# Kernel optimization log

Measured on AMD Instinct MI355X. Metric: run time of the kernel, lower is better.

## Reference

```python
import jax, jax.numpy as jnp
import numpy as np
from jax import lax

BN_EPS = 1e-5
LN_EPS = 1e-5
EPS = 1e-6


def _bn(x, g, b, m, v):
    inv = g / jnp.sqrt(v + BN_EPS)
    return (x - m[None, :, None, None]) * inv[None, :, None, None] + b[None, :, None, None]


def _conv1x1(x, w, b=None):
    y = jnp.einsum('bchw,oc->bohw', x, w)
    if b is not None:
        y = y + b[None, :, None, None]
    return y


def _conv2d(x, w, pad_h, pad_w):
    return lax.conv_general_dilated(x, w, (1, 1), [(pad_h, pad_h), (pad_w, pad_w)],
                                    dimension_numbers=('NCHW', 'OIHW', 'NCHW'))


def _haar_dwt(x):
    # Haar analysis, stride-2: pure 2x2 add/sub arithmetic (H, W assumed even).
    B, C, H, W = x.shape
    xb = x.reshape(B, C, H // 2, 2, W // 2, 2)
    x00 = xb[:, :, :, 0, :, 0]; x01 = xb[:, :, :, 0, :, 1]
    x10 = xb[:, :, :, 1, :, 0]; x11 = xb[:, :, :, 1, :, 1]
    LL = 0.5 * (x00 + x01 + x10 + x11)
    LH = 0.5 * (-x00 + x01 - x10 + x11)
    HL = 0.5 * (-x00 - x01 + x10 + x11)
    HH = 0.5 * (x00 - x01 - x10 + x11)
    return LH, HL, HH, LL


def _haar_idwt(LH, HL, HH, LL):
    # Matches conv_transpose2d(stride=2) with the same Haar kernels.
    x00 = 0.5 * (LL - LH - HL + HH); x01 = 0.5 * (LL + LH - HL - HH)
    x10 = 0.5 * (LL - LH + HL - HH); x11 = 0.5 * (LL + LH + HL + HH)
    B, C, h, w = LL.shape
    top = jnp.stack([x00, x01], axis=-1)  # (B,C,h,w,2)
    bot = jnp.stack([x10, x11], axis=-1)
    y = jnp.stack([top, bot], axis=3)     # (B,C,h,2,w,2)
    return y.reshape(B, C, 2 * h, 2 * w)


def _soft_threshold(x, thr):
    return jnp.sign(x) * jax.nn.relu(jnp.abs(x) - thr)


def _forward(x, red_w, red_bias, red_bn_g, red_bn_b, red_bn_m, red_bn_v,
             gct_fc1_w, gct_fc1_b, gct_ln_g, gct_ln_b, gct_fc2_w, gct_fc2_b,
             rel_h_w, rel_h_b, rel_h_bn_g, rel_h_bn_b, rel_h_bn_m, rel_h_bn_v,
             rel_v_w, rel_v_b, rel_v_bn_g, rel_v_bn_b, rel_v_bn_m, rel_v_bn_v,
             rel_fus_w, rel_fus_b, hw_theta, hw_fuse_w, hw_fc_w, hw_fc_b,
             sf_w, sf_b, sf_bn_g, sf_bn_b, sf_bn_m, sf_bn_v, fin_w, fin_b):
    B, C, H, W = x.shape
    split = C // 2  # alpha = 0.5
    identity = x[:, :split]
    gate = x[:, split:]
    r = jax.nn.relu(_bn(_conv1x1(gate, red_w, red_bias), red_bn_g, red_bn_b, red_bn_m, red_bn_v))
    # --- GCT stream: GAP -> Linear -> LayerNorm -> ReLU -> Linear -> sigmoid gate ---
    ctx = r.mean(axis=(2, 3))                      # (B,Cr)
    h1 = ctx @ gct_fc1_w.T + gct_fc1_b
    mu = h1.mean(-1, keepdims=True)
    var = ((h1 - mu) ** 2).mean(-1, keepdims=True)
    h1 = (h1 - mu) / jnp.sqrt(var + LN_EPS) * gct_ln_g + gct_ln_b
    w_gct = jax.nn.sigmoid(jax.nn.relu(h1) @ gct_fc2_w.T + gct_fc2_b)
    gct_out = r * w_gct[:, :, None, None]
    # --- Rel stream: anisotropic pool -> conv/BN/ReLU -> bilinear(size-1 axis == broadcast) ---
    hf = _conv2d(r.mean(axis=2, keepdims=True), rel_h_w, 0, 1) + rel_h_b[None, :, None, None]
    hf = jax.nn.relu(_bn(hf, rel_h_bn_g, rel_h_bn_b, rel_h_bn_m, rel_h_bn_v))
    hf = jnp.broadcast_to(hf, (B, hf.shape[1], H, W))
    vf = _conv2d(r.mean(axis=3, keepdims=True), rel_v_w, 1, 0) + rel_v_b[None, :, None, None]
    vf = jax.nn.relu(_bn(vf, rel_v_bn_g, rel_v_bn_b, rel_v_bn_m, rel_v_bn_v))
    vf = jnp.broadcast_to(vf, (B, vf.shape[1], H, W))
    rel_w_map = jax.nn.sigmoid(_conv1x1(jnp.concatenate([hf, vf], axis=1), rel_fus_w, rel_fus_b))
    rel_out = r * rel_w_map
    # --- HWFE / wavelet attention ---
    LH, HL, HH, LL = _haar_dwt(r)
    t = jax.nn.sigmoid(hw_theta)                   # (3,Cr,1,1)
    m_LH = jnp.abs(LH).mean(axis=(2, 3), keepdims=True) + EPS
    m_HL = jnp.abs(HL).mean(axis=(2, 3), keepdims=True) + EPS
    m_HH = jnp.abs(HH).mean(axis=(2, 3), keepdims=True) + EPS
    LH_h = _soft_threshold(LH, t[0][None] * m_LH)
    HL_h = _soft_threshold(HL, t[1][None] * m_HL)
    HH_h = _soft_threshold(HH, t[2][None] * m_HH)
    fused = _conv1x1(jnp.concatenate([LH_h, HL_h, HH_h], axis=1), hw_fuse_w)
    X_re = _haar_idwt(LH_h, HL_h, fused, LL)       # note: fused sits in HH slot, as in source
    gap = X_re.mean(axis=(2, 3)) @ hw_fc_w.T + hw_fc_b
    attn = jax.nn.softmax(gap, axis=1)
    hwfe_out = r * attn[:, :, None, None]
    # --- stream fusion + gating ---
    interaction = gct_out * rel_out + hwfe_out
    gate_weight = jax.nn.sigmoid(_bn(_conv1x1(interaction, sf_w, sf_b), sf_bn_g, sf_bn_b, sf_bn_m, sf_bn_v))
    out = jnp.concatenate([identity, gate * gate_weight], axis=1)
    return _conv1x1(out, fin_w, fin_b)


def setup_inputs() -> dict:
    key = jax.random.key(0)
    ks = jax.random.split(key, 20)
    B, C, H, W = 16, 512, 64, 64
    Cg = C // 2           # gate channels = 256
    Cr = 16               # max(4, 256 // 16)
    Ch = Cr // 2          # 8
    Hd = max(1, Cr // 4)  # 4
    f = lambda k, s: jax.random.normal(k, s, jnp.float32) * 0.05
    return dict(
        x=jax.random.normal(ks[0], (B, C, H, W), jnp.float32),
        red_w=f(ks[1], (Cr, Cg)), red_bias=f(ks[2], (Cr,)),
        red_bn_g=jnp.ones((Cr,)), red_bn_b=jnp.zeros((Cr,)),
        red_bn_m=jnp.zeros((Cr,)), red_bn_v=jnp.ones((Cr,)),
        gct_fc1_w=f(ks[3], (Hd, Cr)), gct_fc1_b=f(ks[4], (Hd,)),
        gct_ln_g=jnp.ones((Hd,)), gct_ln_b=jnp.zeros((Hd,)),
        gct_fc2_w=f(ks[5], (Cr, Hd)), gct_fc2_b=f(ks[6], (Cr,)),
        rel_h_w=f(ks[7], (Ch, Cr, 1, 3)), rel_h_b=f(ks[8], (Ch,)),
        rel_h_bn_g=jnp.ones((Ch,)), rel_h_bn_b=jnp.zeros((Ch,)),
        rel_h_bn_m=jnp.zeros((Ch,)), rel_h_bn_v=jnp.ones((Ch,)),
        rel_v_w=f(ks[9], (Ch, Cr, 3, 1)), rel_v_b=f(ks[10], (Ch,)),
        rel_v_bn_g=jnp.ones((Ch,)), rel_v_bn_b=jnp.zeros((Ch,)),
        rel_v_bn_m=jnp.zeros((Ch,)), rel_v_bn_v=jnp.ones((Ch,)),
        rel_fus_w=f(ks[11], (Cr, 2 * Ch)), rel_fus_b=f(ks[12], (Cr,)),
        hw_theta=f(ks[13], (3, Cr, 1, 1)), hw_fuse_w=f(ks[14], (Cr, 3 * Cr)),
        hw_fc_w=f(ks[15], (Cr, Cr)), hw_fc_b=f(ks[16], (Cr,)),
        sf_w=f(ks[17], (Cg, Cr)), sf_b=f(ks[18], (Cg,)),
        sf_bn_g=jnp.ones((Cg,)), sf_bn_b=jnp.zeros((Cg,)),
        sf_bn_m=jnp.zeros((Cg,)), sf_bn_v=jnp.ones((Cg,)),
        fin_w=f(ks[19], (C, C)), fin_b=jnp.zeros((C,)),
    )


def reference(x, red_w, red_bias, red_bn_g, red_bn_b, red_bn_m, red_bn_v,
              gct_fc1_w, gct_fc1_b, gct_ln_g, gct_ln_b, gct_fc2_w, gct_fc2_b,
              rel_h_w, rel_h_b, rel_h_bn_g, rel_h_bn_b, rel_h_bn_m, rel_h_bn_v,
              rel_v_w, rel_v_b, rel_v_bn_g, rel_v_bn_b, rel_v_bn_m, rel_v_bn_v,
              rel_fus_w, rel_fus_b, hw_theta, hw_fuse_w, hw_fc_w, hw_fc_b,
              sf_w, sf_b, sf_bn_g, sf_bn_b, sf_bn_m, sf_bn_v, fin_w, fin_b):
    return _forward(x, red_w, red_bias, red_bn_g, red_bn_b, red_bn_m, red_bn_v,
                    gct_fc1_w, gct_fc1_b, gct_ln_g, gct_ln_b, gct_fc2_w, gct_fc2_b,
                    rel_h_w, rel_h_b, rel_h_bn_g, rel_h_bn_b, rel_h_bn_m, rel_h_bn_v,
                    rel_v_w, rel_v_b, rel_v_bn_g, rel_v_bn_b, rel_v_bn_m, rel_v_bn_v,
                    rel_fus_w, rel_fus_b, hw_theta, hw_fuse_w, hw_fc_w, hw_fc_b,
                    sf_w, sf_b, sf_bn_g, sf_bn_b, sf_bn_m, sf_bn_v, fin_w, fin_b)
```

## Files before the change

kernel.cpp:

```cpp
#include <hip/hip_runtime.h>
#include <cstdint>

typedef uint16_t u16;
typedef uint32_t u32;
typedef uint64_t u64;
typedef __attribute__((ext_vector_type(4))) float f32x4;
typedef __attribute__((ext_vector_type(8))) short bf16x8;

__device__ __forceinline__ u16 f2bf(float f) {
  union { float f; u32 i; } u; u.f = f;
  u32 r = u.i + 0x7FFFu + ((u.i >> 16) & 1u);
  return (u16)(r >> 16);
}
__device__ __forceinline__ float sigm(float x) { return 1.f / (1.f + __expf(-x)); }

__global__ __launch_bounds__(256, 4) void k1_reduce(
    const float* __restrict__ x, const float* __restrict__ rw, const float* __restrict__ rb,
    const float* __restrict__ bg, const float* __restrict__ bb, const float* __restrict__ bm,
    const float* __restrict__ bv, float* __restrict__ r)
{
  __shared__ __align__(16) float wl[256][16];
  __shared__ float bl[16];
  __shared__ float sl[16];
  __shared__ float sc[4][64][17];
  int t = threadIdx.x;
  if (t < 16) {
    float s = bg[t] * rsqrtf(bv[t] + 1e-5f);
    sl[t] = s;
    bl[t] = (rb[t] - bm[t]) * s + bb[t];
  }
  __syncthreads();
  for (int i = 0; i < 16; ++i) {
    int flat = i * 256 + t;
    int co = flat >> 8, c = flat & 255;
    wl[c][co] = rw[co * 256 + c] * sl[co];
  }
  __syncthreads();
  int g = t >> 6, l = t & 63;
  int pg = blockIdx.x * 64 + l;
  int b = pg >> 12, pp = pg & 4095;
  const float* gsrc = x + ((size_t)(b * 512 + 256 + g * 64)) * 4096 + pp;
  float acc[16];
#pragma unroll
  for (int co = 0; co < 16; ++co) acc[co] = 0.f;
#pragma unroll 8
  for (int c = 0; c < 64; ++c) {
    float gv = gsrc[(size_t)c * 4096];
    const f32x4* wr = (const f32x4*)(&wl[g * 64 + c][0]);
    f32x4 a0 = wr[0], a1 = wr[1], a2 = wr[2], a3 = wr[3];
    acc[0]  += gv * a0[0]; acc[1]  += gv * a0[1]; acc[2]  += gv * a0[2]; acc[3]  += gv * a0[3];
    acc[4]  += gv * a1[0]; acc[5]  += gv * a1[1]; acc[6]  += gv * a1[2]; acc[7]  += gv * a1[3];
    acc[8]  += gv * a2[0]; acc[9]  += gv * a2[1]; acc[10] += gv * a2[2]; acc[11] += gv * a2[3];
    acc[12] += gv * a3[0]; acc[13] += gv * a3[1]; acc[14] += gv * a3[2]; acc[15] += gv * a3[3];
  }
#pragma unroll
  for (int co = 0; co < 16; ++co) sc[g][l][co] = acc[co];
  __syncthreads();
  int ppb = (blockIdx.x * 64) & 4095;
#pragma unroll
  for (int i = 0; i < 4; ++i) {
    int idx = i * 256 + t;
    int l2 = idx & 63, co = idx >> 6;
    float s = sc[0][l2][co] + sc[1][l2][co] + sc[2][l2][co] + sc[3][l2][co] + bl[co];
    r[((size_t)(b * 16 + co)) * 4096 + ppb + l2] = fmaxf(s, 0.f);
  }
}

__global__ __launch_bounds__(256) void k2_means(
    const float* __restrict__ r, float* __restrict__ cm, float* __restrict__ rm,
    float* __restrict__ ctx)
{
  __shared__ __align__(16) float tile[64][68];
  int bc = blockIdx.x, t = threadIdx.x;
  const float* src = r + (size_t)bc * 4096;
#pragma unroll
  for (int i = 0; i < 4; ++i) {
    int off = (i * 256 + t) * 4;
    int row = off >> 6, col = off & 63;
    f32x4 v = *(const f32x4*)(src + off);
    *(f32x4*)&tile[row][col] = v;
  }
  __syncthreads();
  int wv = t >> 6, lane = t & 63;
  if (wv == 0) {
    float s = 0.f;
    for (int h = 0; h < 64; ++h) s += tile[h][lane];
    cm[bc * 64 + lane] = s * (1.f / 64.f);
    float tot = s;
#pragma unroll
    for (int m = 32; m; m >>= 1) tot += __shfl_xor(tot, m, 64);
    if (lane == 0) ctx[bc] = tot * (1.f / 4096.f);
  } else if (wv == 1) {
    float s = 0.f;
    for (int w0 = 0; w0 < 64; ++w0) s += tile[lane][(w0 + lane) & 63];
    rm[bc * 64 + lane] = s * (1.f / 64.f);
  }
}

__global__ __launch_bounds__(256) void k3x(
    const float* __restrict__ finw, u16* __restrict__ fwb,
    const float* __restrict__ ctx,
    const float* f1w, const float* f1b, const float* lng, const float* lnb,
    const float* f2w, const float* f2b, const float* fcw, const float* fcb,
    float* __restrict__ wgct, float* __restrict__ attn,
    const float* __restrict__ cm, const float* __restrict__ rm,
    const float* hw, const float* hb, const float* hbg, const float* hbb, const float* hbm, const float* hbv,
    const float* vw, const float* vb_, const float* vbg, const float* vbb, const float* vbm, const float* vbv,
    const float* fw, const float* fb, float* __restrict__ hfc, float* __restrict__ vfc)
{
  int bid = blockIdx.x, t = threadIdx.x;
  if (bid < 256) {
    int i = bid * 256 + t;
    f32x4 v = ((const f32x4*)finw)[i];
    u64 p = (u64)f2bf(v[0]) | ((u64)f2bf(v[1]) << 16) |
            ((u64)f2bf(v[2]) << 32) | ((u64)f2bf(v[3]) << 48);
    ((u64*)fwb)[i] = p;
  } else if (bid == 256) {
    __shared__ float cl[256];
    __shared__ float gl[256];
    cl[t] = ctx[t];
    __syncthreads();
    int b = t >> 4, c = t & 15;
    const float* cb = &cl[b * 16];
    float a[4];
#pragma unroll
    for (int j = 0; j < 4; ++j) {
      float s = f1b[j];
      for (int i = 0; i < 16; ++i) s += cb[i] * f1w[j * 16 + i];
      a[j] = s;
    }
    float mu = 0.25f * (a[0] + a[1] + a[2] + a[3]);
    float var = 0.f;
#pragma unroll
    for (int j = 0; j < 4; ++j) { float d = a[j] - mu; var += d * d; }
    var *= 0.25f;
    float inv = rsqrtf(var + 1e-5f);
#pragma unroll
    for (int j = 0; j < 4; ++j)
      a[j] = fmaxf((a[j] - mu) * inv * lng[j] + lnb[j], 0.f);
    float s2 = f2b[c];
#pragma unroll
    for (int j = 0; j < 4; ++j) s2 += a[j] * f2w[c * 4 + j];
    wgct[t] = sigm(s2);
    float g = fcb[c];
    for (int i = 0; i < 16; ++i) g += cb[i] * fcw[c * 16 + i];
    gl[t] = g;
    __syncthreads();
    const float* gb = &gl[b * 16];
    float mx = -1e30f;
    for (int i = 0; i < 16; ++i) mx = fmaxf(mx, gb[i]);
    float den = 0.f;
    for (int i = 0; i < 16; ++i) den += __expf(gb[i] - mx);
    attn[t] = __expf(g - mx) / den;
  } else {
    __shared__ float cml[16][64], rml[16][64];
    int b = bid - 257;
#pragma unroll
    for (int i = 0; i < 4; ++i) {
      int idx = i * 256 + t;
      int row = idx >> 6, col = idx & 63;
      cml[row][col] = cm[(b * 16 + row) * 64 + col];
      rml[row][col] = rm[(b * 16 + row) * 64 + col];
    }
    __syncthreads();
    if (t < 64) {
      float hf[8], vf[8];
      for (int o = 0; o < 8; ++o) {
        float sh = 0.f, sv = 0.f;
        for (int ci = 0; ci < 16; ++ci) {
#pragma unroll
          for (int kk = 0; kk < 3; ++kk) {
            int q = t + kk - 1;
            bool ok = (q >= 0 && q < 64);
            int qi = ok ? q : 0;
            float xh = ok ? cml[ci][qi] : 0.f;
            float xv = ok ? rml[ci][qi] : 0.f;
            sh += hw[(o * 16 + ci) * 3 + kk] * xh;
            sv += vw[(o * 16 + ci) * 3 + kk] * xv;
          }
        }
        float s1 = hbg[o] * rsqrtf(hbv[o] + 1e-5f);
        hf[o] = fmaxf((sh + hb[o] - hbm[o]) * s1 + hbb[o], 0.f);
        float s2 = vbg[o] * rsqrtf(vbv[o] + 1e-5f);
        vf[o] = fmaxf((sv + vb_[o] - vbm[o]) * s2 + vbb[o], 0.f);
      }
      for (int o = 0; o < 16; ++o) {
        float sh = fb[o], sv = 0.f;
#pragma unroll
        for (int c = 0; c < 8; ++c) {
          sh += fw[o * 16 + c] * hf[c];
          sv += fw[o * 16 + 8 + c] * vf[c];
        }
        hfc[(b * 16 + o) * 64 + t] = sh;
        vfc[(b * 16 + o) * 64 + t] = sv;
      }
    }
  }
}

__global__ __launch_bounds__(512, 4) void k45_v4(
    const float* __restrict__ x, const float* __restrict__ r,
    const float* __restrict__ wgct, const float* __restrict__ attn,
    const float* __restrict__ hfc, const float* __restrict__ vfc,
    const float* __restrict__ sfw, const float* __restrict__ sfb,
    const float* __restrict__ sg, const float* __restrict__ sb_,
    const float* __restrict__ sbm, const float* __restrict__ sbv,
    const u16* __restrict__ fwb, const float* __restrict__ fb,
    float* __restrict__ out)
{
  __shared__ __align__(16) u16 A[64 * 528];
  char* Ab = (char*)A;

  int bid = blockIdx.x;
  int b = bid >> 6, h = bid & 63;
  int t = threadIdx.x;
  int lane = t & 63, wv = t >> 6;

  if (t < 256) {
    int o = t;
    int orow = o & 63, ov = (orow & 7) << 4, ohi = o >> 6;
    float s = sg[o] * rsqrtf(sbv[o] + 1e-5f);
    const f32x4* sw = (const f32x4*)(sfw + o * 16);
    char* rbase = Ab + orow * 1056;
#pragma unroll
    for (int j = 0; j < 4; ++j)
      *(f32x4*)(rbase + ((512 + ohi * 64 + j * 16) ^ ov)) = sw[j] * s;
    *(float*)(rbase + ((768 + ohi * 4) ^ ov)) =
        (sfb[o] - sbm[o]) * s + sb_[o];
  }
#pragma unroll
  for (int i = 0; i < 2; ++i) {
    int idx = i * 512 + t;
    int k = idx >> 6, w = idx & 63;
    float rv = r[((size_t)(b * 16 + k)) * 4096 + h * 64 + w];
    float rel = sigm(hfc[(b * 16 + k) * 64 + w] + vfc[(b * 16 + k) * 64 + h]);
    *(float*)(Ab + w * 1056 + ((784 + k * 4) ^ ((w & 7) << 4))) =
        rv * rv * wgct[b * 16 + k] * rel + rv * attn[b * 16 + k];
  }
  __syncthreads();

  {
    int w = t & 63, og = t >> 6;
    int wx = (w & 7) << 4;
    const char* irow = Ab + w * 1056;
    f32x4 iv0 = *(const f32x4*)(irow + ((784 +  0) ^ wx));
    f32x4 iv1 = *(const f32x4*)(irow + ((784 + 16) ^ wx));
    f32x4 iv2 = *(const f32x4*)(irow + ((784 + 32) ^ wx));
    f32x4 iv3 = *(const f32x4*)(irow + ((784 + 48) ^ wx));
    const float* gsrc = x + ((size_t)(b * 512 + 256)) * 4096 + h * 64 + w;
#pragma unroll
    for (int jo = 0; jo < 4; ++jo) {
      bf16x8 vb;
#pragma unroll
      for (int jj = 0; jj < 8; ++jj) {
        int o = og * 32 + jo * 8 + jj;
        int orow = o & 63, ov = (orow & 7) << 4, ohi = o >> 6;
        const char* rbase = Ab + orow * 1056;
        f32x4 w0 = *(const f32x4*)(rbase + ((512 + ohi * 64 +  0) ^ ov));
        f32x4 w1 = *(const f32x4*)(rbase + ((512 + ohi * 64 + 16) ^ ov));
        f32x4 w2 = *(const f32x4*)(rbase + ((512 + ohi * 64 + 32) ^ ov));
        f32x4 w3 = *(const f32x4*)(rbase + ((512 + ohi * 64 + 48) ^ ov));
        float dot = *(const float*)(rbase + ((768 + ohi * 4) ^ ov));
        dot += iv0[0] * w0[0] + iv0[1] * w0[1] + iv0[2] * w0[2] + iv0[3] * w0[3];
        dot += iv1[0] * w1[0] + iv1[1] * w1[1] + iv1[2] * w1[2] + iv1[3] * w1[3];
        dot += iv2[0] * w2[0] + iv2[1] * w2[1] + iv2[2] * w2[2] + iv2[3] * w2[3];
        dot += iv3[0] * w3[0] + iv3[1] * w3[1] + iv3[2] * w3[2] + iv3[3] * w3[3];
        float gwv = sigm(dot);
        float gv = gsrc[(size_t)o * 4096];
        vb[jj] = (short)f2bf(gv * gwv);
      }
      *(bf16x8*)(Ab + w * 1056 + ((og * 64 + jo * 16) ^ wx)) = vb;
    }
  }
  __syncthreads();

  {
    int q = lane & 15, cg = lane >> 4;
    int m = q * 4 + cg;
    int mx = (m & 7) << 4;
#pragma unroll
    for (int i = 0; i < 4; ++i) {
      int cbase = i * 64 + wv * 8;
      f32x4 vA = *(const f32x4*)(x + ((size_t)(b * 512 + cbase + cg)) * 4096 + h * 64 + q * 4);
      f32x4 vB = *(const f32x4*)(x + ((size_t)(b * 512 + cbase + 4 + cg)) * 4096 + h * 64 + q * 4);
      u32 a01 = (u32)f2bf(vA[0]) | ((u32)f2bf(vA[1]) << 16);
      u32 a23 = (u32)f2bf(vA[2]) | ((u32)f2bf(vA[3]) << 16);
      u32 b01 = (u32)f2bf(vB[0]) | ((u32)f2bf(vB[1]) << 16);
      u32 b23 = (u32)f2bf(vB[2]) | ((u32)f2bf(vB[3]) << 16);
      int jp = cg;
      u32 e[8];
#pragma unroll
      for (int cp = 0; cp < 4; ++cp) {
        int srcaddr = (cp * 16 + q) << 2;
        u32 rA01 = (u32)__builtin_amdgcn_ds_bpermute(srcaddr, (int)a01);
        u32 rA23 = (u32)__builtin_amdgcn_ds_bpermute(srcaddr, (int)a23);
        u32 rB01 = (u32)__builtin_amdgcn_ds_bpermute(srcaddr, (int)b01);
        u32 rB23 = (u32)__builtin_amdgcn_ds_bpermute(srcaddr, (int)b23);
        u32 selA = (jp < 2) ? rA01 : rA23;
        u32 selB = (jp < 2) ? rB01 : rB23;
        e[cp]     = (jp & 1) ? (selA >> 16) : (selA & 0xffffu);
        e[4 + cp] = (jp & 1) ? (selB >> 16) : (selB & 0xffffu);
      }
      bf16x8 pk;
#pragma unroll
      for (int j = 0; j < 8; ++j) pk[j] = (short)e[j];
      *(bf16x8*)(Ab + m * 1056 + ((512 + i * 128 + wv * 16) ^ mx)) = pk;
    }
  }
  __syncthreads();

  int fr = lane & 15, quad = lane >> 4;
  int fx = (fr & 7) << 4;
  int n0w = wv * 64;
  f32x4 acc[4][4];
#pragma unroll
  for (int j = 0; j < 4; ++j) {
    float bvv = fb[n0w + j * 16 + fr];
    f32x4 b4 = {bvv, bvv, bvv, bvv};
#pragma unroll
    for (int i = 0; i < 4; ++i) acc[i][j] = b4;
  }
  const u16* Bp = fwb + (size_t)(n0w + fr) * 512 + quad * 8;
  for (int kb = 0; kb < 16; ++kb) {
    int kbb = kb ^ 8;
    bf16x8 af[4], bfr[4];
#pragma unroll
    for (int i = 0; i < 4; ++i)
      af[i] = *(const bf16x8*)(Ab + (size_t)(i * 16 + fr) * 1056 +
                               ((kb * 64 + quad * 16) ^ fx));
#pragma unroll
    for (int j = 0; j < 4; ++j)
      bfr[j] = *(const bf16x8*)(Bp + (size_t)(j * 16) * 512 + kbb * 32);
#pragma unroll
    for (int j = 0; j < 4; ++j)
#pragma unroll
      for (int i = 0; i < 4; ++i)
        acc[i][j] = __builtin_amdgcn_mfma_f32_16x16x32_bf16(af[i], bfr[j], acc[i][j], 0, 0, 0);
  }

  float* ob = out + ((size_t)(b * 512 + n0w + fr)) * 4096 + h * 64 + quad * 4;
#pragma unroll
  for (int j = 0; j < 4; ++j)
#pragma unroll
    for (int i = 0; i < 4; ++i)
      *(f32x4*)(ob + (size_t)(j * 16) * 4096 + i * 16) = acc[i][j];
}

extern "C" void kernel_launch(void* const* d_in, const int* in_sizes, int n_in,
                              void* d_out, int out_size, void* d_ws, size_t ws_size,
                              hipStream_t stream) {
  const float* x      = (const float*)d_in[0];
  const float* red_w  = (const float*)d_in[1];
  const float* red_b  = (const float*)d_in[2];
  const float* rbg    = (const float*)d_in[3];
  const float* rbb    = (const float*)d_in[4];
  const float* rbm    = (const float*)d_in[5];
  const float* rbv    = (const float*)d_in[6];
  const float* f1w    = (const float*)d_in[7];
  const float* f1b    = (const float*)d_in[8];
  const float* lng    = (const float*)d_in[9];
  const float* lnb    = (const float*)d_in[10];
  const float* f2w    = (const float*)d_in[11];
  const float* f2b    = (const float*)d_in[12];
  const float* rhw    = (const float*)d_in[13];
  const float* rhb    = (const float*)d_in[14];
  const float* rhbg   = (const float*)d_in[15];
  const float* rhbb   = (const float*)d_in[16];
  const float* rhbm   = (const float*)d_in[17];
  const float* rhbv   = (const float*)d_in[18];
  const float* rvw    = (const float*)d_in[19];
  const float* rvb    = (const float*)d_in[20];
  const float* rvbg   = (const float*)d_in[21];
  const float* rvbb   = (const float*)d_in[22];
  const float* rvbm   = (const float*)d_in[23];
  const float* rvbv   = (const float*)d_in[24];
  const float* fusw   = (const float*)d_in[25];
  const float* fusb   = (const float*)d_in[26];
  const float* fcw    = (const float*)d_in[29];
  const float* fcb    = (const float*)d_in[30];
  const float* sfw    = (const float*)d_in[31];
  const float* sfb    = (const float*)d_in[32];
  const float* sbg    = (const float*)d_in[33];
  const float* sbb    = (const float*)d_in[34];
  const float* sbm    = (const float*)d_in[35];
  const float* sbv    = (const float*)d_in[36];
  const float* finw   = (const float*)d_in[37];
  const float* finb   = (const float*)d_in[38];
  float* out = (float*)d_out;

  char* ws = (char*)d_ws;
  size_t off = 0;
  float* r   = (float*)(ws + off); off += (size_t)16 * 16 * 4096 * 4;
  u16*   fwb = (u16*)(ws + off);   off += (size_t)512 * 512 * 2;
  float* cm  = (float*)(ws + off); off += 65536;
  float* rm  = (float*)(ws + off); off += 65536;
  float* ctx = (float*)(ws + off); off += 1024;
  float* wg  = (float*)(ws + off); off += 1024;
  float* at  = (float*)(ws + off); off += 1024;
  float* hfc = (float*)(ws + off); off += 65536;
  float* vfc = (float*)(ws + off); off += 65536;

  k1_reduce<<<1024, 256, 0, stream>>>(x, red_w, red_b, rbg, rbb, rbm, rbv, r);
  k2_means<<<256, 256, 0, stream>>>(r, cm, rm, ctx);
  k3x<<<273, 256, 0, stream>>>(finw, fwb,
                               ctx, f1w, f1b, lng, lnb, f2w, f2b, fcw, fcb, wg, at,
                               cm, rm, rhw, rhb, rhbg, rhbb, rhbm, rhbv,
                               rvw, rvb, rvbg, rvbb, rvbm, rvbv, fusw, fusb, hfc, vfc);
  k45_v4<<<1024, 512, 0, stream>>>(x, r, wg, at, hfc, vfc,
                                   sfw, sfb, sbg, sbb, sbm, sbv, fwb, finb, out);
}
```

Measured before the change: 401.1 us.

## Hoist global loads of x early and precompute sf BN fold in k3x

Moves the BN scale/shift fold for the sf conv out of every k45 block into a one-time computation in k3x, stored in a small workspace buffer. In k45, all global loads of the identity half and the gate values of x are issued at kernel start into registers, so their latency overlaps the intermediate computation. The sf weights are now read from global/scalar memory with a wave-uniform index instead of being staged in LDS, which removes one barrier. The cost is much higher register pressure (32 gate floats plus 8 float4s per thread) under the 512x4 launch bound, with a risk of spills or lower occupancy.

```diff
diff --git a/kernel.cpp b/kernel.cpp
--- a/kernel.cpp
+++ b/kernel.cpp
@@ -106,7 +106,9 @@
     const float* __restrict__ cm, const float* __restrict__ rm,
     const float* hw, const float* hb, const float* hbg, const float* hbb, const float* hbm, const float* hbv,
     const float* vw, const float* vb_, const float* vbg, const float* vbb, const float* vbm, const float* vbv,
-    const float* fw, const float* fb, float* __restrict__ hfc, float* __restrict__ vfc)
+    const float* fw, const float* fb, float* __restrict__ hfc, float* __restrict__ vfc,
+    const float* __restrict__ sfb2, const float* __restrict__ sbg2, const float* __restrict__ sbb2,
+    const float* __restrict__ sbm2, const float* __restrict__ sbv2, float* __restrict__ sb2)
 {
   int bid = blockIdx.x, t = threadIdx.x;
   if (bid < 256) {
@@ -116,6 +118,11 @@
             ((u64)f2bf(v[2]) << 32) | ((u64)f2bf(v[3]) << 48);
     ((u64*)fwb)[i] = p;
   } else if (bid == 256) {
+    {
+      float s = sbg2[t] * rsqrtf(sbv2[t] + 1e-5f);
+      sb2[2 * t]     = s;
+      sb2[2 * t + 1] = (sfb2[t] - sbm2[t]) * s + sbb2[t];
+    }
     __shared__ float cl[256];
     __shared__ float gl[256];
     cl[t] = ctx[t];
@@ -198,96 +205,56 @@
   }
 }
 
-__global__ __launch_bounds__(512, 4) void k45_v4(
+__global__ __launch_bounds__(512, 4) void k45_v5(
     const float* __restrict__ x, const float* __restrict__ r,
     const float* __restrict__ wgct, const float* __restrict__ attn,
     const float* __restrict__ hfc, const float* __restrict__ vfc,
-    const float* __restrict__ sfw, const float* __restrict__ sfb,
-    const float* __restrict__ sg, const float* __restrict__ sb_,
-    const float* __restrict__ sbm, const float* __restrict__ sbv,
+    const float* __restrict__ sfw, const float* __restrict__ sb2,
     const u16* __restrict__ fwb, const float* __restrict__ fb,
     float* __restrict__ out)
 {
   __shared__ __align__(16) u16 A[64 * 528];
+  __shared__ float intr[16][68];
   char* Ab = (char*)A;
 
   int bid = blockIdx.x;
   int b = bid >> 6, h = bid & 63;
   int t = threadIdx.x;
   int lane = t & 63, wv = t >> 6;
-
-  if (t < 256) {
-    int o = t;
-    int orow = o & 63, ov = (orow & 7) << 4, ohi = o >> 6;
-    float s = sg[o] * rsqrtf(sbv[o] + 1e-5f);
-    const f32x4* sw = (const f32x4*)(sfw + o * 16);
-    char* rbase = Ab + orow * 1056;
-#pragma unroll
-    for (int j = 0; j < 4; ++j)
-      *(f32x4*)(rbase + ((512 + ohi * 64 + j * 16) ^ ov)) = sw[j] * s;
-    *(float*)(rbase + ((768 + ohi * 4) ^ ov)) =
-        (sfb[o] - sbm[o]) * s + sb_[o];
+  int q = lane & 15, cg = lane >> 4;
+  int w = t & 63, og = t >> 6;
+
+  f32x4 idA[4], idB[4];
+#pragma unroll
+  for (int i = 0; i < 4; ++i) {
+    int cbase = i * 64 + wv * 8;
+    idA[i] = *(const f32x4*)(x + ((size_t)(b * 512 + cbase + cg)) * 4096 + h * 64 + q * 4);
+    idB[i] = *(const f32x4*)(x + ((size_t)(b * 512 + cbase + 4 + cg)) * 4096 + h * 64 + q * 4);
+  }
+  float gvp[32];
+  {
+    const float* gsrc = x + ((size_t)(b * 512 + 256 + og * 32)) * 4096 + h * 64 + w;
+#pragma unroll
+    for (int j = 0; j < 32; ++j) gvp[j] = gsrc[(size_t)j * 4096];
   }
 #pragma unroll
   for (int i = 0; i < 2; ++i) {
     int idx = i * 512 + t;
-    int k = idx >> 6, w = idx & 63;
-    float rv = r[((size_t)(b * 16 + k)) * 4096 + h * 64 + w];
-    float rel = sigm(hfc[(b * 16 + k) * 64 + w] + vfc[(b * 16 + k) * 64 + h]);
-    *(float*)(Ab + w * 1056 + ((784 + k * 4) ^ ((w & 7) << 4))) =
-        rv * rv * wgct[b * 16 + k] * rel + rv * attn[b * 16 + k];
-  }
-  __syncthreads();
-
+    int k = idx >> 6, ww = idx & 63;
+    float rv = r[((size_t)(b * 16 + k)) * 4096 + h * 64 + ww];
+    float rel = sigm(hfc[(b * 16 + k) * 64 + ww] + vfc[(b * 16 + k) * 64 + h]);
+    intr[k][ww] = rv * rv * wgct[b * 16 + k] * rel + rv * attn[b * 16 + k];
+  }
   {
-    int w = t & 63, og = t >> 6;
-    int wx = (w & 7) << 4;
-    const char* irow = Ab + w * 1056;
-    f32x4 iv0 = *(const f32x4*)(irow + ((784 +  0) ^ wx));
-    f32x4 iv1 = *(const f32x4*)(irow + ((784 + 16) ^ wx));
-    f32x4 iv2 = *(const f32x4*)(irow + ((784 + 32) ^ wx));
-    f32x4 iv3 = *(const f32x4*)(irow + ((784 + 48) ^ wx));
-    const float* gsrc = x + ((size_t)(b * 512 + 256)) * 4096 + h * 64 + w;
-#pragma unroll
-    for (int jo = 0; jo < 4; ++jo) {
-      bf16x8 vb;
-#pragma unroll
-      for (int jj = 0; jj < 8; ++jj) {
-        int o = og * 32 + jo * 8 + jj;
-        int orow = o & 63, ov = (orow & 7) << 4, ohi = o >> 6;
-        const char* rbase = Ab + orow * 1056;
-        f32x4 w0 = *(const f32x4*)(rbase + ((512 + ohi * 64 +  0) ^ ov));
-        f32x4 w1 = *(const f32x4*)(rbase + ((512 + ohi * 64 + 16) ^ ov));
-        f32x4 w2 = *(const f32x4*)(rbase + ((512 + ohi * 64 + 32) ^ ov));
-        f32x4 w3 = *(const f32x4*)(rbase + ((512 + ohi * 64 + 48) ^ ov));
-        float dot = *(const float*)(rbase + ((768 + ohi * 4) ^ ov));
-        dot += iv0[0] * w0[0] + iv0[1] * w0[1] + iv0[2] * w0[2] + iv0[3] * w0[3];
-        dot += iv1[0] * w1[0] + iv1[1] * w1[1] + iv1[2] * w1[2] + iv1[3] * w1[3];
-        dot += iv2[0] * w2[0] + iv2[1] * w2[1] + iv2[2] * w2[2] + iv2[3] * w2[3];
-        dot += iv3[0] * w3[0] + iv3[1] * w3[1] + iv3[2] * w3[2] + iv3[3] * w3[3];
-        float gwv = sigm(dot);
-        float gv = gsrc[(size_t)o * 4096];
-        vb[jj] = (short)f2bf(gv * gwv);
-      }
-      *(bf16x8*)(Ab + w * 1056 + ((og * 64 + jo * 16) ^ wx)) = vb;
-    }
-  }
-  __syncthreads();
-
-  {
-    int q = lane & 15, cg = lane >> 4;
     int m = q * 4 + cg;
     int mx = (m & 7) << 4;
+    int jp = cg;
 #pragma unroll
     for (int i = 0; i < 4; ++i) {
-      int cbase = i * 64 + wv * 8;
-      f32x4 vA = *(const f32x4*)(x + ((size_t)(b * 512 + cbase + cg)) * 4096 + h * 64 + q * 4);
-      f32x4 vB = *(const f32x4*)(x + ((size_t)(b * 512 + cbase + 4 + cg)) * 4096 + h * 64 + q * 4);
-      u32 a01 = (u32)f2bf(vA[0]) | ((u32)f2bf(vA[1]) << 16);
-      u32 a23 = (u32)f2bf(vA[2]) | ((u32)f2bf(vA[3]) << 16);
-      u32 b01 = (u32)f2bf(vB[0]) | ((u32)f2bf(vB[1]) << 16);
-      u32 b23 = (u32)f2bf(vB[2]) | ((u32)f2bf(vB[3]) << 16);
-      int jp = cg;
+      u32 a01 = (u32)f2bf(idA[i][0]) | ((u32)f2bf(idA[i][1]) << 16);
+      u32 a23 = (u32)f2bf(idA[i][2]) | ((u32)f2bf(idA[i][3]) << 16);
+      u32 b01 = (u32)f2bf(idB[i][0]) | ((u32)f2bf(idB[i][1]) << 16);
+      u32 b23 = (u32)f2bf(idB[i][2]) | ((u32)f2bf(idB[i][3]) << 16);
       u32 e[8];
 #pragma unroll
       for (int cp = 0; cp < 4; ++cp) {
@@ -303,8 +270,35 @@
       }
       bf16x8 pk;
 #pragma unroll
-      for (int j = 0; j < 8; ++j) pk[j] = (short)e[j];
+      for (int j2 = 0; j2 < 8; ++j2) pk[j2] = (short)e[j2];
       *(bf16x8*)(Ab + m * 1056 + ((512 + i * 128 + wv * 16) ^ mx)) = pk;
+    }
+  }
+  __syncthreads();
+
+  {
+    int wx = (w & 7) << 4;
+    int ogu = __builtin_amdgcn_readfirstlane(og);
+    float iv[16];
+#pragma unroll
+    for (int k2 = 0; k2 < 16; ++k2) iv[k2] = intr[k2][w];
+#pragma unroll
+    for (int jo = 0; jo < 4; ++jo) {
+      bf16x8 vb;
+#pragma unroll
+      for (int jj = 0; jj < 8; ++jj) {
+        int o = ogu * 32 + jo * 8 + jj;
+        const f32x4* wr = (const f32x4*)(sfw + o * 16);
+        f32x4 w0 = wr[0], w1 = wr[1], w2 = wr[2], w3 = wr[3];
+        float dot = iv[0]  * w0[0] + iv[1]  * w0[1] + iv[2]  * w0[2] + iv[3]  * w0[3]
+                  + iv[4]  * w1[0] + iv[5]  * w1[1] + iv[6]  * w1[2] + iv[7]  * w1[3]
+                  + iv[8]  * w2[0] + iv[9]  * w2[1] + iv[10] * w2[2] + iv[11] * w2[3]
+                  + iv[12] * w3[0] + iv[13] * w3[1] + iv[14] * w3[2] + iv[15] * w3[3];
+        float s_ = sb2[2 * o], bso = sb2[2 * o + 1];
+        float gwv = sigm(dot * s_ + bso);
+        vb[jj] = (short)f2bf(gvp[jo * 8 + jj] * gwv);
+      }
+      *(bf16x8*)(Ab + w * 1056 + ((og * 64 + jo * 16) ^ wx)) = vb;
     }
   }
   __syncthreads();
@@ -399,13 +393,15 @@
   float* at  = (float*)(ws + off); off += 1024;
   float* hfc = (float*)(ws + off); off += 65536;
   float* vfc = (float*)(ws + off); off += 65536;
+  float* sb2 = (float*)(ws + off); off += 2048;
 
   k1_reduce<<<1024, 256, 0, stream>>>(x, red_w, red_b, rbg, rbb, rbm, rbv, r);
   k2_means<<<256, 256, 0, stream>>>(r, cm, rm, ctx);
   k3x<<<273, 256, 0, stream>>>(finw, fwb,
                                ctx, f1w, f1b, lng, lnb, f2w, f2b, fcw, fcb, wg, at,
                                cm, rm, rhw, rhb, rhbg, rhbb, rhbm, rhbv,
-                               rvw, rvb, rvbg, rvbb, rvbm, rvbv, fusw, fusb, hfc, vfc);
-  k45_v4<<<1024, 512, 0, stream>>>(x, r, wg, at, hfc, vfc,
-                                   sfw, sfb, sbg, sbb, sbm, sbv, fwb, finb, out);
-}
+                               rvw, rvb, rvbg, rvbb, rvbm, rvbv, fusw, fusb, hfc, vfc,
+                               sfb, sbg, sbb, sbm, sbv, sb2);
+  k45_v5<<<1024, 512, 0, stream>>>(x, r, wg, at, hfc, vfc,
+                                   sfw, sb2, fwb, finb, out);
+}
```

Measured after the change: 413.9 us. +3.2%, slower.
